# Kernel tuning notes

Measured on AMD Instinct MI355X. Metric: run time of the kernel, lower is better.

## Reference

```python
import jax, jax.numpy as jnp
import numpy as np
from jax import lax

EPS_ACT = 1e-5
EPS_RMS = 1e-6


def _ste(x, q):
    # straight-through estimator: forward = q, backward = identity
    return x + lax.stop_gradient(q - x)


def _act_quant8(x):
    # per-last-dim symmetric 8-bit activation quantization (BitNet style)
    scale = 127.0 / jnp.clip(jnp.max(jnp.abs(x), axis=-1, keepdims=True), EPS_ACT)
    return jnp.clip(jnp.round(x * scale), -128.0, 127.0) / scale


def _w_quant_8bit(w):
    # per-tensor symmetric 8-bit weight quantization
    scale = 127.0 / jnp.clip(jnp.max(jnp.abs(w)), EPS_ACT)
    return jnp.clip(jnp.round(w * scale), -128.0, 127.0) / scale


def _w_quant_binary(w):
    # per-tensor binary: sign(w) * mean(|w|)
    return jnp.sign(w) * jnp.mean(jnp.abs(w))


def _rmsnorm(x):
    return x * lax.rsqrt(jnp.mean(x * x, axis=-1, keepdims=True) + EPS_RMS)


def _bit_conv(x, w, quant_type, groups):
    xq = _ste(x, _act_quant8(x))
    wq = _ste(w, _w_quant_binary(w) if quant_type == 'Binary' else _w_quant_8bit(w))
    return lax.conv_general_dilated(
        xq, wq, window_strides=(1, 1), padding='VALID',
        feature_group_count=groups,
        dimension_numbers=('NCHW', 'OIHW', 'NCHW'))


def _bit_linear(x, w):
    x = _rmsnorm(x)                       # NormType='RMS' (no learned scale)
    xq = _ste(x, _act_quant8(x))
    wq = _ste(w, _w_quant_binary(w))      # QuantType='Binary', per-tensor
    return xq @ wq.T


def setup_inputs() -> dict:
    key = jax.random.key(0)
    ks = jax.random.split(key, 8)
    B = 8192
    return {
        'x':        jax.random.normal(ks[0], (B, 1, 16, 16), jnp.float32),
        'w_conv1':  jax.random.normal(ks[1], (16, 1, 3, 3),  jnp.float32) * 0.1,
        'w_conv1b': jax.random.normal(ks[2], (16, 16, 3, 3), jnp.float32) * 0.1,
        'w_conv2':  jax.random.normal(ks[3], (96, 1, 12, 12), jnp.float32) * 0.1,
        'w_fc1':    jax.random.normal(ks[4], (64, 96), jnp.float32) * 0.1,
        'w_fc2':    jax.random.normal(ks[5], (64, 64), jnp.float32) * 0.1,
        'w_fc3':    jax.random.normal(ks[6], (64, 64), jnp.float32) * 0.1,
        'w_fcl':    jax.random.normal(ks[7], (10, 64), jnp.float32) * 0.1,
    }


def reference(x, w_conv1, w_conv1b, w_conv2, w_fc1, w_fc2, w_fc3, w_fcl):
    h = jax.nn.relu(_bit_conv(x, w_conv1, '8bit', 1))        # [B,16,14,14]
    h = jax.nn.relu(_bit_conv(h, w_conv1b, '8bit', 1))       # [B,16,12,12]
    h = jax.nn.relu(_bit_conv(h, w_conv2, 'Binary', 16))     # [B,96,1,1]
    h = h.reshape(h.shape[0], -1)                            # [B,96]
    h = jax.nn.relu(_bit_linear(h, w_fc1))                   # [B,64]
    h = jax.nn.relu(_bit_linear(h, w_fc2))                   # [B,64]
    h = jax.nn.relu(_bit_linear(h, w_fc3))                   # [B,64]
    return _bit_linear(h, w_fcl)                             # [B,10]
```

## Files before the change

kernel.cpp:

```cpp
#include <hip/hip_runtime.h>
#include <math.h>


#define OFF_W1   0
#define OFF_W1B  144
#define OFF_W2   2448
#define OFF_F1   16272
#define OFF_F2   22416
#define OFF_F3   26512
#define OFF_FL   30608

#define EPS_TIE  3e-5f

__device__ __forceinline__ float quantq(float v, float s) {
    const float u  = __fmul_rn(v, s);
    const float fl = floorf(u);
    const float fr = __fsub_rn(u, fl);
    float q;
    if (fabsf(__fsub_rn(fr, 0.5f)) < EPS_TIE) q = __fadd_rn(fl, 0.5f);
    else                                      q = rintf(u);
    q = fminf(q, 127.f);
    return __fdiv_rn(q, s);
}

__device__ __forceinline__ float leaf_abs_sum(const float* __restrict__ p, int n) {
    float r[8];
    #pragma unroll
    for (int j = 0; j < 8; ++j) r[j] = fabsf(p[j]);
    const int nb = n & ~7;
    for (int i = 8; i < nb; i += 8) {
        #pragma unroll
        for (int j = 0; j < 8; ++j) r[j] = __fadd_rn(r[j], fabsf(p[i + j]));
    }
    float c = __fadd_rn(__fadd_rn(__fadd_rn(r[0], r[1]), __fadd_rn(r[2], r[3])),
                        __fadd_rn(__fadd_rn(r[4], r[5]), __fadd_rn(r[6], r[7])));
    for (int i = nb; i < n; ++i) c = __fadd_rn(c, fabsf(p[i]));
    return c;
}

__global__ __launch_bounds__(256) void wq_kernel(
    const float* __restrict__ w1, const float* __restrict__ w1b,
    const float* __restrict__ w2, const float* __restrict__ f1,
    const float* __restrict__ f2, const float* __restrict__ f3,
    const float* __restrict__ fl, float* __restrict__ ws)
{
    __shared__ float red[256];
    __shared__ float ls[128];
    const int blk = blockIdx.x, t = threadIdx.x;

    const float* src; int n; int mode; int off; int K; int W;
    switch (blk) {
        case 0:  src = w1;  n = 144;   mode = 0; off = OFF_W1;  K = 0;   W = 0;  break;
        case 1:  src = w1b; n = 2304;  mode = 0; off = OFF_W1B; K = 144; W = 16; break;
        case 2:  src = w2;  n = 13824; mode = 1; off = OFF_W2;  K = 144; W = 96; break;
        case 3:  src = f1;  n = 6144;  mode = 1; off = OFF_F1;  K = 96;  W = 64; break;
        case 4:  src = f2;  n = 4096;  mode = 1; off = OFF_F2;  K = 64;  W = 64; break;
        case 5:  src = f3;  n = 4096;  mode = 1; off = OFF_F3;  K = 64;  W = 64; break;
        default: src = fl;  n = 640;   mode = 1; off = OFF_FL;  K = 64;  W = 10; break;
    }

    if (mode == 0) {
        float p = 0.f;
        for (int i = t; i < n; i += 256) p = fmaxf(p, fabsf(src[i]));
        red[t] = p;
        __syncthreads();
        for (int s = 128; s > 0; s >>= 1) {
            if (t < s) red[t] = fmaxf(red[t], red[t + s]);
            __syncthreads();
        }
        const float s = __fdiv_rn(127.0f, fmaxf(red[0], 1e-5f));
        for (int i = t; i < n; i += 256) {
            float q = rintf(__fmul_rn(src[i], s));
            q = fminf(fmaxf(q, -128.f), 127.f);
            const int d = (K == 0) ? i : (i % K) * W + (i / K);
            ws[off + d] = __fdiv_rn(q, s);
        }
    } else {
        int nleaf, loff, lsz;
        switch (n) {
            case 13824: nleaf = 128; loff = (t >> 1) * 216 + (t & 1) * 104;
                        lsz = (t & 1) ? 112 : 104; break;
            case 6144:  nleaf = 64;  loff = t * 96;  lsz = 96;  break;
            case 4096:  nleaf = 32;  loff = t * 128; lsz = 128; break;
            default:    nleaf = 8;   loff = t * 80;  lsz = 80;  break;
        }
        if (t < nleaf) ls[t] = leaf_abs_sum(src + loff, lsz);
        __syncthreads();
        for (int m = nleaf >> 1; m >= 1; m >>= 1) {
            float v = 0.f;
            if (t < m) v = __fadd_rn(ls[2 * t], ls[2 * t + 1]);
            __syncthreads();
            if (t < m) ls[t] = v;
            __syncthreads();
        }
        const float alpha = __fdiv_rn(ls[0], (float)n);
        for (int i = t; i < n; i += 256) {
            const float w = src[i];
            const float sg = (w > 0.f) ? 1.f : ((w < 0.f) ? -1.f : 0.f);
            const int d = (i % K) * W + (i / K);
            ws[off + d] = __fmul_rn(sg, alpha);
        }
    }
}

__global__ __launch_bounds__(256) void fused_kernel(
    const float* __restrict__ x, const float* __restrict__ ws,
    float* __restrict__ out)
{
    __shared__ float s_w1[144];
    __shared__ float s_w1bT[2304];
    __shared__ float s_x[16][17];
    __shared__ float s_h1[16][14][17];
    __shared__ float s_h2[16][12][17];
    __shared__ float s_v96[96];
    __shared__ float s_t96[96];
    __shared__ float s_q[96];
    __shared__ float s_v64[64];
    __shared__ float s_r8[8];
    __shared__ float s_bc;

    const int b = blockIdx.x;
    const int t = threadIdx.x;

    for (int i = t; i < 144;  i += 256) s_w1[i]   = ws[OFF_W1 + i];
    for (int i = t; i < 2304; i += 256) s_w1bT[i] = ws[OFF_W1B + i];

    {
        const float v = x[b * 256 + t];
        float m = fabsf(v);
        #pragma unroll
        for (int msk = 8; msk >= 1; msk >>= 1) m = fmaxf(m, __shfl_xor(m, msk, 16));
        const float s = __fdiv_rn(127.0f, fmaxf(m, 1e-5f));
        float q = rintf(__fmul_rn(v, s));
        q = fminf(fmaxf(q, -128.f), 127.f);
        s_x[t >> 4][t & 15] = __fdiv_rn(q, s);
    }
    __syncthreads();

    if (t < 224) {
        const int oc = t / 14, oh = t % 14;
        float w[9];
        #pragma unroll
        for (int k = 0; k < 9; ++k) w[k] = s_w1[oc * 9 + k];
        float row[14], mx = 0.f;
        #pragma unroll
        for (int ow = 0; ow < 14; ++ow) {
            float acc = 0.f;
            #pragma unroll
            for (int kh = 0; kh < 3; ++kh)
                #pragma unroll
                for (int kw = 0; kw < 3; ++kw)
                    acc = __fmaf_rn(s_x[oh + kh][ow + kw], w[kh * 3 + kw], acc);
            acc = fmaxf(acc, 0.f);
            row[ow] = acc; mx = fmaxf(mx, acc);
        }
        const float s = __fdiv_rn(127.0f, fmaxf(mx, 1e-5f));
        #pragma unroll
        for (int ow = 0; ow < 14; ++ow)
            s_h1[oc][oh][ow] = quantq(row[ow], s);
    }
    __syncthreads();

    if (t < 192) {
        const int oc = t / 12, oh = t % 12;
        float acc[12];
        #pragma unroll
        for (int i = 0; i < 12; ++i) acc[i] = 0.f;
        for (int ic = 0; ic < 16; ++ic) {
            #pragma unroll
            for (int kh = 0; kh < 3; ++kh) {
                float A[14];
                #pragma unroll
                for (int j = 0; j < 14; ++j) A[j] = s_h1[ic][oh + kh][j];
                #pragma unroll
                for (int kw = 0; kw < 3; ++kw) {
                    const float w = s_w1bT[(ic * 9 + kh * 3 + kw) * 16 + oc];
                    #pragma unroll
                    for (int ow = 0; ow < 12; ++ow)
                        acc[ow] = __fmaf_rn(A[ow + kw], w, acc[ow]);
                }
            }
        }
        float mx = 0.f;
        #pragma unroll
        for (int ow = 0; ow < 12; ++ow) { acc[ow] = fmaxf(acc[ow], 0.f); mx = fmaxf(mx, acc[ow]); }
        const float s = __fdiv_rn(127.0f, fmaxf(mx, 1e-5f));
        #pragma unroll
        for (int ow = 0; ow < 12; ++ow)
            s_h2[oc][oh][ow] = quantq(acc[ow], s);
    }
    __syncthreads();

    if (t < 96) {
        const int g = t / 6;
        const float* wp = ws + OFF_W2;
        float acc = 0.f;
        #pragma unroll
        for (int r = 0; r < 12; ++r)
            #pragma unroll
            for (int c = 0; c < 12; ++c)
                acc = __fmaf_rn(s_h2[g][r][c], wp[(r * 12 + c) * 96 + t], acc);
        s_v96[t] = fmaxf(acc, 0.f);
    }
    __syncthreads();

    if (t < 96) s_t96[t] = __fmul_rn(s_v96[t], s_v96[t]);
    __syncthreads();
    if (t < 8) {
        float r = s_t96[t];
        for (int i = 8; i < 96; i += 8) r = __fadd_rn(r, s_t96[i + t]);
        s_r8[t] = r;
    }
    __syncthreads();
    if (t == 0) {
        const float c = __fadd_rn(
            __fadd_rn(__fadd_rn(s_r8[0], s_r8[1]), __fadd_rn(s_r8[2], s_r8[3])),
            __fadd_rn(__fadd_rn(s_r8[4], s_r8[5]), __fadd_rn(s_r8[6], s_r8[7])));
        const float mean = __fdiv_rn(c, 96.0f);
        s_bc = __fdiv_rn(1.0f, __fsqrt_rn(__fadd_rn(mean, 1e-6f)));
    }
    __syncthreads();
    if (t < 96) s_t96[t] = __fmul_rn(s_v96[t], s_bc);
    __syncthreads();
    if (t < 64) {
        float m = s_t96[t];
        if (t < 32) m = fmaxf(m, s_t96[64 + t]);
        #pragma unroll
        for (int msk = 32; msk >= 1; msk >>= 1) m = fmaxf(m, __shfl_xor(m, msk, 64));
        if (t == 0) s_bc = __fdiv_rn(127.0f, fmaxf(m, 1e-5f));
    }
    __syncthreads();
    if (t < 96) s_q[t] = quantq(s_t96[t], s_bc);
    __syncthreads();
    if (t < 64) {
        const float* wp = ws + OFF_F1;
        float acc = 0.f;
        for (int k = 0; k < 96; ++k) acc = __fmaf_rn(s_q[k], wp[k * 64 + t], acc);
        s_v64[t] = fmaxf(acc, 0.f);
    }
    __syncthreads();

    #pragma unroll 1
    for (int stage = 0; stage < 2; ++stage) {
        const int woff = stage == 0 ? OFF_F2 : OFF_F3;
        if (t < 64) s_t96[t] = __fmul_rn(s_v64[t], s_v64[t]);
        __syncthreads();
        if (t < 8) {
            float r = s_t96[t];
            for (int i = 8; i < 64; i += 8) r = __fadd_rn(r, s_t96[i + t]);
            s_r8[t] = r;
        }
        __syncthreads();
        if (t == 0) {
            const float c = __fadd_rn(
                __fadd_rn(__fadd_rn(s_r8[0], s_r8[1]), __fadd_rn(s_r8[2], s_r8[3])),
                __fadd_rn(__fadd_rn(s_r8[4], s_r8[5]), __fadd_rn(s_r8[6], s_r8[7])));
            const float mean = __fdiv_rn(c, 64.0f);
            s_bc = __fdiv_rn(1.0f, __fsqrt_rn(__fadd_rn(mean, 1e-6f)));
        }
        __syncthreads();
        if (t < 64) s_t96[t] = __fmul_rn(s_v64[t], s_bc);
        __syncthreads();
        if (t < 64) {
            float m = s_t96[t];
            #pragma unroll
            for (int msk = 32; msk >= 1; msk >>= 1) m = fmaxf(m, __shfl_xor(m, msk, 64));
            if (t == 0) s_bc = __fdiv_rn(127.0f, fmaxf(m, 1e-5f));
        }
        __syncthreads();
        if (t < 64) s_q[t] = quantq(s_t96[t], s_bc);
        __syncthreads();
        if (t < 64) {
            const float* wp = ws + woff;
            float acc = 0.f;
            for (int k = 0; k < 64; ++k) acc = __fmaf_rn(s_q[k], wp[k * 64 + t], acc);
            s_v64[t] = fmaxf(acc, 0.f);
        }
        __syncthreads();
    }

    if (t < 64) s_t96[t] = __fmul_rn(s_v64[t], s_v64[t]);
    __syncthreads();
    if (t < 8) {
        float r = s_t96[t];
        for (int i = 8; i < 64; i += 8) r = __fadd_rn(r, s_t96[i + t]);
        s_r8[t] = r;
    }
    __syncthreads();
    if (t == 0) {
        const float c = __fadd_rn(
            __fadd_rn(__fadd_rn(s_r8[0], s_r8[1]), __fadd_rn(s_r8[2], s_r8[3])),
            __fadd_rn(__fadd_rn(s_r8[4], s_r8[5]), __fadd_rn(s_r8[6], s_r8[7])));
        const float mean = __fdiv_rn(c, 64.0f);
        s_bc = __fdiv_rn(1.0f, __fsqrt_rn(__fadd_rn(mean, 1e-6f)));
    }
    __syncthreads();
    if (t < 64) s_t96[t] = __fmul_rn(s_v64[t], s_bc);
    __syncthreads();
    if (t < 64) {
        float m = s_t96[t];
        #pragma unroll
        for (int msk = 32; msk >= 1; msk >>= 1) m = fmaxf(m, __shfl_xor(m, msk, 64));
        if (t == 0) s_bc = __fdiv_rn(127.0f, fmaxf(m, 1e-5f));
    }
    __syncthreads();
    if (t < 64) s_q[t] = quantq(s_t96[t], s_bc);
    __syncthreads();
    if (t < 10) {
        const float* wp = ws + OFF_FL;
        float acc = 0.f;
        for (int k = 0; k < 64; ++k) acc = __fmaf_rn(s_q[k], wp[k * 10 + t], acc);
        out[b * 10 + t] = acc;
    }
}

extern "C" void kernel_launch(void* const* d_in, const int* in_sizes, int n_in,
                              void* d_out, int out_size, void* d_ws, size_t ws_size,
                              hipStream_t stream) {
    const float* x   = (const float*)d_in[0];
    const float* w1  = (const float*)d_in[1];
    const float* w1b = (const float*)d_in[2];
    const float* w2  = (const float*)d_in[3];
    const float* f1  = (const float*)d_in[4];
    const float* f2  = (const float*)d_in[5];
    const float* f3  = (const float*)d_in[6];
    const float* fl  = (const float*)d_in[7];
    float* out = (float*)d_out;
    float* ws  = (float*)d_ws;

    const int B = in_sizes[0] / 256;

    wq_kernel<<<7, 256, 0, stream>>>(w1, w1b, w2, f1, f2, f3, fl, ws);
    fused_kernel<<<B, 256, 0, stream>>>(x, ws, out);
}
```

Before: 265.5 us.

## Read conv weights from global in padded layout and vectorize LDS accesses

Conv1 and conv1b weights are no longer staged into shared memory per block. Instead they are stored per output channel in a 12-float-padded layout, so each thread reads them directly from global memory with float4 loads. Shared activation tiles are padded to 20 floats per row and 16-byte aligned so rows can be read and written with float4 and float2 LDS operations. Conv1 is restructured to load each input row into registers once and reuse it across kernel taps. The trade-off is more global or cache traffic for weights in exchange for less LDS staging and fewer LDS instructions, plus possible bank conflicts from the new row stride.

Result: no change. 264.4 us (-0.4%).

```diff
diff --git a/kernel.cpp b/kernel.cpp
--- a/kernel.cpp
+++ b/kernel.cpp
@@ -3,12 +3,12 @@
 
 
 #define OFF_W1   0
-#define OFF_W1B  144
-#define OFF_W2   2448
-#define OFF_F1   16272
-#define OFF_F2   22416
-#define OFF_F3   26512
-#define OFF_FL   30608
+#define OFF_W1B  192
+#define OFF_W2   3264
+#define OFF_F1   17088
+#define OFF_F2   23232
+#define OFF_F3   27328
+#define OFF_FL   31424
 
 #define EPS_TIE  3e-5f
 
@@ -51,7 +51,7 @@
     const float* src; int n; int mode; int off; int K; int W;
     switch (blk) {
         case 0:  src = w1;  n = 144;   mode = 0; off = OFF_W1;  K = 0;   W = 0;  break;
-        case 1:  src = w1b; n = 2304;  mode = 0; off = OFF_W1B; K = 144; W = 16; break;
+        case 1:  src = w1b; n = 2304;  mode = 0; off = OFF_W1B; K = 0;   W = 0;  break;
         case 2:  src = w2;  n = 13824; mode = 1; off = OFF_W2;  K = 144; W = 96; break;
         case 3:  src = f1;  n = 6144;  mode = 1; off = OFF_F1;  K = 96;  W = 64; break;
         case 4:  src = f2;  n = 4096;  mode = 1; off = OFF_F2;  K = 64;  W = 64; break;
@@ -72,7 +72,10 @@
         for (int i = t; i < n; i += 256) {
             float q = rintf(__fmul_rn(src[i], s));
             q = fminf(fmaxf(q, -128.f), 127.f);
-            const int d = (K == 0) ? i : (i % K) * W + (i / K);
+            int d;
+            if (blk == 0) d = (i / 9) * 12 + (i % 9);
+            else          { const int oc = i / 144, k = i % 144;
+                            d = oc * 192 + (k / 9) * 12 + (k % 9); }
             ws[off + d] = __fdiv_rn(q, s);
         }
     } else {
@@ -107,11 +110,9 @@
     const float* __restrict__ x, const float* __restrict__ ws,
     float* __restrict__ out)
 {
-    __shared__ float s_w1[144];
-    __shared__ float s_w1bT[2304];
-    __shared__ float s_x[16][17];
-    __shared__ float s_h1[16][14][17];
-    __shared__ float s_h2[16][12][17];
+    __shared__ __align__(16) float s_x[16][20];
+    __shared__ __align__(16) float s_h1[16][14][20];
+    __shared__ __align__(16) float s_h2[16][12][20];
     __shared__ float s_v96[96];
     __shared__ float s_t96[96];
     __shared__ float s_q[96];
@@ -122,9 +123,6 @@
     const int b = blockIdx.x;
     const int t = threadIdx.x;
 
-    for (int i = t; i < 144;  i += 256) s_w1[i]   = ws[OFF_W1 + i];
-    for (int i = t; i < 2304; i += 256) s_w1bT[i] = ws[OFF_W1B + i];
-
     {
         const float v = x[b * 256 + t];
         float m = fabsf(v);
@@ -139,42 +137,65 @@
 
     if (t < 224) {
         const int oc = t / 14, oh = t % 14;
-        float w[9];
-        #pragma unroll
-        for (int k = 0; k < 9; ++k) w[k] = s_w1[oc * 9 + k];
-        float row[14], mx = 0.f;
-        #pragma unroll
-        for (int ow = 0; ow < 14; ++ow) {
-            float acc = 0.f;
-            #pragma unroll
-            for (int kh = 0; kh < 3; ++kh)
+        const float* __restrict__ wg = ws + OFF_W1 + oc * 12;
+        const float4 wv0 = *(const float4*)&wg[0];
+        const float4 wv1 = *(const float4*)&wg[4];
+        const float  w8  = wg[8];
+        const float w[9] = {wv0.x, wv0.y, wv0.z, wv0.w,
+                            wv1.x, wv1.y, wv1.z, wv1.w, w8};
+        float acc[14];
+        #pragma unroll
+        for (int ow = 0; ow < 14; ++ow) acc[ow] = 0.f;
+        #pragma unroll
+        for (int kh = 0; kh < 3; ++kh) {
+            float A[16];
+            #pragma unroll
+            for (int j4 = 0; j4 < 4; ++j4)
+                *(float4*)&A[j4 * 4] = *(const float4*)&s_x[oh + kh][j4 * 4];
+            #pragma unroll
+            for (int kw = 0; kw < 3; ++kw) {
+                const float wk = w[kh * 3 + kw];
                 #pragma unroll
-                for (int kw = 0; kw < 3; ++kw)
-                    acc = __fmaf_rn(s_x[oh + kh][ow + kw], w[kh * 3 + kw], acc);
-            acc = fmaxf(acc, 0.f);
-            row[ow] = acc; mx = fmaxf(mx, acc);
-        }
+                for (int ow = 0; ow < 14; ++ow)
+                    acc[ow] = __fmaf_rn(A[ow + kw], wk, acc[ow]);
+            }
+        }
+        float mx = 0.f;
+        #pragma unroll
+        for (int ow = 0; ow < 14; ++ow) { acc[ow] = fmaxf(acc[ow], 0.f); mx = fmaxf(mx, acc[ow]); }
         const float s = __fdiv_rn(127.0f, fmaxf(mx, 1e-5f));
-        #pragma unroll
-        for (int ow = 0; ow < 14; ++ow)
-            s_h1[oc][oh][ow] = quantq(row[ow], s);
+        float q[14];
+        #pragma unroll
+        for (int ow = 0; ow < 14; ++ow) q[ow] = quantq(acc[ow], s);
+        *(float4*)&s_h1[oc][oh][0]  = *(const float4*)&q[0];
+        *(float4*)&s_h1[oc][oh][4]  = *(const float4*)&q[4];
+        *(float4*)&s_h1[oc][oh][8]  = *(const float4*)&q[8];
+        *(float2*)&s_h1[oc][oh][12] = *(const float2*)&q[12];
     }
     __syncthreads();
 
     if (t < 192) {
         const int oc = t / 12, oh = t % 12;
+        const float* __restrict__ wg = ws + OFF_W1B + oc * 192;
         float acc[12];
         #pragma unroll
         for (int i = 0; i < 12; ++i) acc[i] = 0.f;
         for (int ic = 0; ic < 16; ++ic) {
+            const float4 wv0 = *(const float4*)&wg[ic * 12];
+            const float4 wv1 = *(const float4*)&wg[ic * 12 + 4];
+            const float  w8  = wg[ic * 12 + 8];
+            const float wr[9] = {wv0.x, wv0.y, wv0.z, wv0.w,
+                                 wv1.x, wv1.y, wv1.z, wv1.w, w8};
             #pragma unroll
             for (int kh = 0; kh < 3; ++kh) {
                 float A[14];
-                #pragma unroll
-                for (int j = 0; j < 14; ++j) A[j] = s_h1[ic][oh + kh][j];
+                *(float4*)&A[0]  = *(const float4*)&s_h1[ic][oh + kh][0];
+                *(float4*)&A[4]  = *(const float4*)&s_h1[ic][oh + kh][4];
+                *(float4*)&A[8]  = *(const float4*)&s_h1[ic][oh + kh][8];
+                *(float2*)&A[12] = *(const float2*)&s_h1[ic][oh + kh][12];
                 #pragma unroll
                 for (int kw = 0; kw < 3; ++kw) {
-                    const float w = s_w1bT[(ic * 9 + kh * 3 + kw) * 16 + oc];
+                    const float w = wr[kh * 3 + kw];
                     #pragma unroll
                     for (int ow = 0; ow < 12; ++ow)
                         acc[ow] = __fmaf_rn(A[ow + kw], w, acc[ow]);
@@ -185,21 +206,29 @@
         #pragma unroll
         for (int ow = 0; ow < 12; ++ow) { acc[ow] = fmaxf(acc[ow], 0.f); mx = fmaxf(mx, acc[ow]); }
         const float s = __fdiv_rn(127.0f, fmaxf(mx, 1e-5f));
-        #pragma unroll
-        for (int ow = 0; ow < 12; ++ow)
-            s_h2[oc][oh][ow] = quantq(acc[ow], s);
+        float q[12];
+        #pragma unroll
+        for (int ow = 0; ow < 12; ++ow) q[ow] = quantq(acc[ow], s);
+        *(float4*)&s_h2[oc][oh][0] = *(const float4*)&q[0];
+        *(float4*)&s_h2[oc][oh][4] = *(const float4*)&q[4];
+        *(float4*)&s_h2[oc][oh][8] = *(const float4*)&q[8];
     }
     __syncthreads();
 
     if (t < 96) {
         const int g = t / 6;
-        const float* wp = ws + OFF_W2;
+        const float* __restrict__ wp = ws + OFF_W2;
         float acc = 0.f;
         #pragma unroll
-        for (int r = 0; r < 12; ++r)
+        for (int r = 0; r < 12; ++r) {
+            float A[12];
+            *(float4*)&A[0] = *(const float4*)&s_h2[g][r][0];
+            *(float4*)&A[4] = *(const float4*)&s_h2[g][r][4];
+            *(float4*)&A[8] = *(const float4*)&s_h2[g][r][8];
             #pragma unroll
             for (int c = 0; c < 12; ++c)
-                acc = __fmaf_rn(s_h2[g][r][c], wp[(r * 12 + c) * 96 + t], acc);
+                acc = __fmaf_rn(A[c], wp[(r * 12 + c) * 96 + t], acc);
+        }
         s_v96[t] = fmaxf(acc, 0.f);
     }
     __syncthreads();
@@ -233,7 +262,7 @@
     if (t < 96) s_q[t] = quantq(s_t96[t], s_bc);
     __syncthreads();
     if (t < 64) {
-        const float* wp = ws + OFF_F1;
+        const float* __restrict__ wp = ws + OFF_F1;
         float acc = 0.f;
         for (int k = 0; k < 96; ++k) acc = __fmaf_rn(s_q[k], wp[k * 64 + t], acc);
         s_v64[t] = fmaxf(acc, 0.f);
@@ -271,7 +300,7 @@
         if (t < 64) s_q[t] = quantq(s_t96[t], s_bc);
         __syncthreads();
         if (t < 64) {
-            const float* wp = ws + woff;
+            const float* __restrict__ wp = ws + woff;
             float acc = 0.f;
             for (int k = 0; k < 64; ++k) acc = __fmaf_rn(s_q[k], wp[k * 64 + t], acc);
             s_v64[t] = fmaxf(acc, 0.f);
@@ -307,7 +336,7 @@
     if (t < 64) s_q[t] = quantq(s_t96[t], s_bc);
     __syncthreads();
     if (t < 10) {
-        const float* wp = ws + OFF_FL;
+        const float* __restrict__ wp = ws + OFF_FL;
         float acc = 0.f;
         for (int k = 0; k < 64; ++k) acc = __fmaf_rn(s_q[k], wp[k * 10 + t], acc);
         out[b * 10 + t] = acc;
```
